# Kernel tuning notes

Hardware: AMD Instinct MI355X
Metric: run time of the kernel (lower is better)

Reference implementation:

```python
import jax, jax.numpy as jnp
import numpy as np

LN_EPS = 1e-5


def _layernorm(x, w, b):
    mu = jnp.mean(x, axis=-1, keepdims=True)
    var = jnp.mean((x - mu) ** 2, axis=-1, keepdims=True)
    return (x - mu) * jax.lax.rsqrt(var + LN_EPS) * w + b


def setup_inputs() -> dict:
    key = jax.random.key(0)
    n, d = 512, 256
    ks = jax.random.split(key, 12)
    s = 1.0 / np.sqrt(d)
    inp = {
        "h": jax.random.normal(ks[0], (n, d), dtype=jnp.float32),
        "e": jax.random.normal(ks[1], (n, n, d), dtype=jnp.float32),
        "t_emb": jax.random.normal(ks[2], (d,), dtype=jnp.float32),
        "W1": jax.random.uniform(ks[3], (d, d), jnp.float32, -s, s),
        "W2": jax.random.uniform(ks[4], (d, d), jnp.float32, -s, s),
        "W3": jax.random.uniform(ks[5], (d, d), jnp.float32, -s, s),
        "W_t": jax.random.uniform(ks[6], (d, d), jnp.float32, -s, s),
        "W4": jax.random.uniform(ks[7], (d, d), jnp.float32, -s, s),
        "W5": jax.random.uniform(ks[8], (d, d), jnp.float32, -s, s),
        "gate_w": jax.random.uniform(ks[9], (d, 1), jnp.float32, -s, s),
        "gate_b": jax.random.uniform(ks[10], (1,), jnp.float32, -s, s),
        "ln_e_w": jnp.ones((d,), jnp.float32),
        "ln_e_b": jnp.zeros((d,), jnp.float32),
        "ln_h_w": jnp.ones((d,), jnp.float32),
        "ln_h_b": jnp.zeros((d,), jnp.float32),
    }
    return inp


def reference(h, e, t_emb, W1, W2, W3, W_t, W4, W5, gate_w, gate_b,
              ln_e_w, ln_e_b, ln_h_w, ln_h_b):
    # nn.Linear applies x @ W.T (no bias except gate)
    t_bias = t_emb @ W_t.T                      # (d,)
    hi = (h @ W1.T)[:, None, :]                 # (n,1,d)
    hj = (h @ W2.T)[None, :, :]                 # (1,n,d)
    pre = hi + hj + jnp.einsum('ijd,kd->ijk', e, W3) + t_bias  # (n,n,d)
    e_new = jax.nn.relu(_layernorm(pre, ln_e_w, ln_e_b))       # (n,n,d)
    logits = e_new @ gate_w + gate_b            # (n,n,1)
    eta = jax.nn.softmax(logits, axis=1)        # softmax over j (dim=1)
    agg = jnp.einsum('ijk,ijd,kd->ik', eta * 1.0, e_new, W5) if False else \
          jnp.sum(eta * jnp.einsum('ijd,kd->ijk', e_new, W5), axis=1)  # (n,d)
    h_new = h + jax.nn.relu(_layernorm(h @ W4.T + agg, ln_h_w, ln_h_b))
    return (h_new, e_new)
```

## Files before the change

kernel.cpp:

```cpp
#include <hip/hip_runtime.h>

#define NN 512
#define DD 256

typedef float f32x4 __attribute__((ext_vector_type(4)));
typedef short s16x8 __attribute__((ext_vector_type(8)));

__device__ __forceinline__ unsigned short f2bf(float f) {
    unsigned u = __float_as_uint(f);
    u += 0x7fffu + ((u >> 16) & 1u);
    return (unsigned short)(u >> 16);
}
__device__ __forceinline__ float bf2f(unsigned short s) {
    return __uint_as_float(((unsigned)s) << 16);
}

__global__ __launch_bounds__(256) void k1_pre(
    const float* __restrict__ h,  const float* __restrict__ W1,
    const float* __restrict__ W2, const float* __restrict__ W4,
    const float* __restrict__ t_emb, const float* __restrict__ W_t,
    const float* __restrict__ W3,
    float* __restrict__ hb, float* __restrict__ hW2, float* __restrict__ hW4,
    unsigned short* __restrict__ w3b,
    float* __restrict__ wacc, float* __restrict__ zacc)
{
    __shared__ float xs[8][DD];
    __shared__ float st[DD];
    const int b = blockIdx.x;
    const int t = threadIdx.x;
    if (b < 64) {
        #pragma unroll
        for (int r = 0; r < 8; ++r) xs[r][t] = h[(size_t)(b * 8 + r) * DD + t];
        st[t] = t_emb[t];
        __syncthreads();
        float a1[8], a2[8], a4[8];
        #pragma unroll
        for (int r = 0; r < 8; ++r) { a1[r] = 0.f; a2[r] = 0.f; a4[r] = 0.f; }
        float tb = 0.f;
        for (int d = 0; d < DD; ++d) {
            const float w1 = W1[(size_t)t * DD + d];
            const float w2 = W2[(size_t)t * DD + d];
            const float w4 = W4[(size_t)t * DD + d];
            tb = fmaf(st[d], W_t[(size_t)t * DD + d], tb);
            #pragma unroll
            for (int r = 0; r < 8; ++r) {
                const float x = xs[r][d];
                a1[r] = fmaf(x, w1, a1[r]);
                a2[r] = fmaf(x, w2, a2[r]);
                a4[r] = fmaf(x, w4, a4[r]);
            }
        }
        #pragma unroll
        for (int r = 0; r < 8; ++r) {
            const size_t o = (size_t)(b * 8 + r) * DD + t;
            hb[o] = a1[r] + tb; hW2[o] = a2[r]; hW4[o] = a4[r];
        }
    } else if (b == 64) {
        for (int c = t; c < DD * DD / 4; c += 256) {
            const f32x4 v = *reinterpret_cast<const f32x4*>(W3 + (size_t)c * 4);
            const unsigned lo = ((unsigned)f2bf(v[1]) << 16) | f2bf(v[0]);
            const unsigned hi = ((unsigned)f2bf(v[3]) << 16) | f2bf(v[2]);
            *reinterpret_cast<uint2*>(w3b + (size_t)c * 4) = make_uint2(lo, hi);
        }
    } else {
        const f32x4 zero = (f32x4){0.f, 0.f, 0.f, 0.f};
        for (int c = t; c < NN * DD / 4; c += 256)
            *reinterpret_cast<f32x4*>(wacc + (size_t)c * 4) = zero;
        if (t < 256) { zacc[t] = 0.f; zacc[t + 256] = 0.f; }
    }
}

__global__ __launch_bounds__(256) void k2_big(
    const float* __restrict__ e,
    const unsigned short* __restrict__ w3b,
    const float* __restrict__ hb, const float* __restrict__ hW2,
    const float* __restrict__ gate_w, const float* __restrict__ gate_b,
    const float* __restrict__ ln_e_w, const float* __restrict__ ln_e_b,
    float* __restrict__ out_e,
    float* __restrict__ wacc, float* __restrict__ zacc)
{
    const int b = blockIdx.x;
    const int row_base = b * 32;
    const int i = row_base >> 9;
    const int j0 = row_base & 511;
    const int tid = threadIdx.x;
    const int w = tid >> 6;
    const int l = tid & 63;
    const int l15 = l & 15;
    const int lg = l >> 4;

    __shared__ __align__(16) unsigned char sA[32 * 256 * 2];
    __shared__ __align__(16) unsigned char sH2[32 * 256 * 2];
    __shared__ unsigned short s_hbu[DD];
    __shared__ float s_lnw[DD], s_lnb[DD], s_gw[DD];
    __shared__ float s_part[32][4][2];
    __shared__ float s_glog[32][4];

    const float* esrc = e + (size_t)row_base * DD;
    f32x4 av[8];
    #pragma unroll
    for (int s = 0; s < 8; ++s)
        av[s] = *reinterpret_cast<const f32x4*>(esrc + (size_t)(s * 256 + tid) * 4);

    const unsigned short* bp = w3b + (size_t)(w * 64 + l15) * DD + lg * 8;
    s16x8 bb[4][4];
    #pragma unroll
    for (int kk = 0; kk < 4; ++kk)
        #pragma unroll
        for (int n = 0; n < 4; ++n)
            bb[kk][n] = *reinterpret_cast<const s16x8*>(bp + (size_t)n * 16 * DD + kk * 32);

    const float gb = gate_b[0];
    s_lnw[tid] = ln_e_w[tid];
    s_lnb[tid] = ln_e_b[tid];
    s_gw[tid]  = gate_w[tid];
    s_hbu[tid] = f2bf(hb[(size_t)i * DD + tid]);

    #pragma unroll
    for (int s = 0; s < 8; ++s) {
        const int flat = s * 256 + tid;
        const int r = flat >> 6;
        const int c4 = (flat & 63) * 4;
        const f32x4 v = av[s];
        const unsigned lo = ((unsigned)f2bf(v[1]) << 16) | f2bf(v[0]);
        const unsigned hi = ((unsigned)f2bf(v[3]) << 16) | f2bf(v[2]);
        const unsigned byte = ((unsigned)(r * 512 + c4 * 2)) ^ ((unsigned)(r & 7) << 4);
        *reinterpret_cast<uint2*>(sA + byte) = make_uint2(lo, hi);
    }

    {
        const float* h2src = hW2 + (size_t)j0 * DD;
        f32x4 hv[8];
        #pragma unroll
        for (int s = 0; s < 8; ++s)
            hv[s] = *reinterpret_cast<const f32x4*>(h2src + (size_t)(s * 256 + tid) * 4);
        #pragma unroll
        for (int s = 0; s < 8; ++s) {
            const int flat = s * 256 + tid;
            const int r = flat >> 6;
            const int c4 = (flat & 63) * 4;
            const f32x4 v = hv[s];
            const unsigned lo = ((unsigned)f2bf(v[1]) << 16) | f2bf(v[0]);
            const unsigned hi = ((unsigned)f2bf(v[3]) << 16) | f2bf(v[2]);
            const unsigned byte = ((unsigned)(r * 512 + c4 * 2)) ^ ((unsigned)(r & 7) << 4);
            *reinterpret_cast<uint2*>(sH2 + byte) = make_uint2(lo, hi);
        }
    }
    __syncthreads();

    f32x4 acc[2][4];
    #pragma unroll
    for (int m = 0; m < 2; ++m)
        #pragma unroll
        for (int n = 0; n < 4; ++n)
            acc[m][n] = (f32x4){0.f, 0.f, 0.f, 0.f};

    const unsigned aswz = ((unsigned)(l15 & 7) << 4);
    #pragma unroll
    for (int kk = 0; kk < 8; ++kk) {
        s16x8 afr[2];
        #pragma unroll
        for (int m = 0; m < 2; ++m) {
            const unsigned byte = ((unsigned)((m * 16 + l15) * 512 + kk * 64 + lg * 16)) ^ aswz;
            afr[m] = *reinterpret_cast<const s16x8*>(sA + byte);
        }
        #pragma unroll
        for (int n = 0; n < 4; ++n)
            #pragma unroll
            for (int m = 0; m < 2; ++m)
                acc[m][n] = __builtin_amdgcn_mfma_f32_16x16x32_bf16(afr[m], bb[kk & 3][n], acc[m][n], 0, 0, 0);
        if (kk < 4) {
            #pragma unroll
            for (int n = 0; n < 4; ++n)
                bb[kk & 3][n] = *reinterpret_cast<const s16x8*>(bp + (size_t)n * 16 * DD + (kk + 4) * 32);
        }
    }

    float hbn[4];
    #pragma unroll
    for (int n = 0; n < 4; ++n) hbn[n] = bf2f(s_hbu[w * 64 + n * 16 + l15]);

    #pragma unroll
    for (int m = 0; m < 2; ++m) {
        #pragma unroll
        for (int q = 0; q < 4; ++q) {
            const int r = m * 16 + lg * 4 + q;
            const unsigned rsw = ((unsigned)(r & 7) << 4);
            float s1 = 0.f, s2 = 0.f;
            #pragma unroll
            for (int n = 0; n < 4; ++n) {
                const int c = w * 64 + n * 16 + l15;
                const unsigned short h2u = *reinterpret_cast<const unsigned short*>(
                    sH2 + (((unsigned)(r * 512 + c * 2)) ^ rsw));
                const float v = acc[m][n][q] + hbn[n] + bf2f(h2u);
                acc[m][n][q] = v;
                s1 += v;
                s2 = fmaf(v, v, s2);
            }
            #pragma unroll
            for (int s = 1; s < 16; s <<= 1) {
                s1 += __shfl_xor(s1, s, 64);
                s2 += __shfl_xor(s2, s, 64);
            }
            if (l15 == 0) { s_part[r][w][0] = s1; s_part[r][w][1] = s2; }
        }
    }
    __syncthreads();

    #pragma unroll
    for (int m = 0; m < 2; ++m) {
        #pragma unroll
        for (int q = 0; q < 4; ++q) {
            const int r = m * 16 + lg * 4 + q;
            float S1 = 0.f, S2 = 0.f;
            #pragma unroll
            for (int ww = 0; ww < 4; ++ww) { S1 += s_part[r][ww][0]; S2 += s_part[r][ww][1]; }
            const float mu = S1 * (1.f / 256.f);
            const float rs = rsqrtf(S2 * (1.f / 256.f) - mu * mu + 1e-5f);
            const size_t rowg = (size_t)(row_base + r);
            float gl = 0.f;
            #pragma unroll
            for (int n = 0; n < 4; ++n) {
                const int c = w * 64 + n * 16 + l15;
                float v = (acc[m][n][q] - mu) * rs * s_lnw[c] + s_lnb[c];
                v = fmaxf(v, 0.f);
                acc[m][n][q] = v;
                out_e[rowg * DD + c] = v;
                gl = fmaf(v, s_gw[c], gl);
            }
            #pragma unroll
            for (int s = 1; s < 16; s <<= 1) gl += __shfl_xor(gl, s, 64);
            if (l15 == 0) s_glog[r][w] = gl;
        }
    }
    __syncthreads();

    float p[4] = {0.f, 0.f, 0.f, 0.f};
    float zl = 0.f;
    #pragma unroll
    for (int m = 0; m < 2; ++m) {
        #pragma unroll
        for (int q = 0; q < 4; ++q) {
            const int r = m * 16 + lg * 4 + q;
            const float lv = gb + s_glog[r][0] + s_glog[r][1] + s_glog[r][2] + s_glog[r][3];
            const float ex = __expf(lv);
            zl += ex;
            #pragma unroll
            for (int n = 0; n < 4; ++n) p[n] = fmaf(ex, acc[m][n][q], p[n]);
        }
    }
    #pragma unroll
    for (int n = 0; n < 4; ++n) {
        p[n] += __shfl_xor(p[n], 16, 64);
        p[n] += __shfl_xor(p[n], 32, 64);
    }
    zl += __shfl_xor(zl, 16, 64);
    zl += __shfl_xor(zl, 32, 64);
    if (lg == 0) {
        #pragma unroll
        for (int n = 0; n < 4; ++n)
            atomicAdd(&wacc[(size_t)i * DD + w * 64 + n * 16 + l15], p[n]);
    }
    if (w == 0 && l == 0) atomicAdd(&zacc[i], zl);
}

__global__ __launch_bounds__(256) void k4_final(
    const float* __restrict__ wacc, const float* __restrict__ zacc,
    const float* __restrict__ W5,
    const float* __restrict__ hW4, const float* __restrict__ h,
    const float* __restrict__ ln_h_w, const float* __restrict__ ln_h_b,
    float* __restrict__ out_h)
{
    const int i = blockIdx.x;
    const int k = threadIdx.x;
    __shared__ float xs[DD];
    __shared__ float red[256];

    const float zinv = 1.f / zacc[i];
    xs[k] = wacc[(size_t)i * DD + k] * zinv;
    __syncthreads();
    float a = 0.f;
    for (int d = 0; d < DD; ++d) a = fmaf(xs[d], W5[(size_t)k * DD + d], a);
    const float p = hW4[(size_t)i * DD + k] + a;

    red[k] = p;
    __syncthreads();
    for (int s = 128; s > 0; s >>= 1) {
        if (k < s) red[k] += red[k + s];
        __syncthreads();
    }
    const float mu = red[0] * (1.f / 256.f);
    __syncthreads();
    const float d0 = p - mu;
    red[k] = d0 * d0;
    __syncthreads();
    for (int s = 128; s > 0; s >>= 1) {
        if (k < s) red[k] += red[k + s];
        __syncthreads();
    }
    const float rs = rsqrtf(red[0] * (1.f / 256.f) + 1e-5f);
    float v = d0 * rs * ln_h_w[k] + ln_h_b[k];
    v = fmaxf(v, 0.f);
    out_h[(size_t)i * DD + k] = h[(size_t)i * DD + k] + v;
}

extern "C" void kernel_launch(void* const* d_in, const int* in_sizes, int n_in,
                              void* d_out, int out_size, void* d_ws, size_t ws_size,
                              hipStream_t stream)
{
    const float* h      = (const float*)d_in[0];
    const float* e      = (const float*)d_in[1];
    const float* t_emb  = (const float*)d_in[2];
    const float* W1     = (const float*)d_in[3];
    const float* W2     = (const float*)d_in[4];
    const float* W3     = (const float*)d_in[5];
    const float* W_t    = (const float*)d_in[6];
    const float* W4     = (const float*)d_in[7];
    const float* W5     = (const float*)d_in[8];
    const float* gate_w = (const float*)d_in[9];
    const float* gate_b = (const float*)d_in[10];
    const float* ln_e_w = (const float*)d_in[11];
    const float* ln_e_b = (const float*)d_in[12];
    const float* ln_h_w = (const float*)d_in[13];
    const float* ln_h_b = (const float*)d_in[14];

    float* out_h = (float*)d_out;
    float* out_e = out_h + NN * DD;

    float* wsf  = (float*)d_ws;
    float* hb   = wsf;
    float* hW2  = hb + NN * DD;
    float* hW4  = hW2 + NN * DD;
    float* wacc = hW4 + NN * DD;
    float* zacc = wacc + NN * DD;
    unsigned short* w3b = (unsigned short*)(zacc + NN);

    k1_pre<<<66, 256, 0, stream>>>(h, W1, W2, W4, t_emb, W_t, W3,
                                   hb, hW2, hW4, w3b, wacc, zacc);
    k2_big<<<8192, 256, 0, stream>>>(e, w3b, hb, hW2, gate_w, gate_b,
                                     ln_e_w, ln_e_b, out_e, wacc, zacc);
    k4_final<<<512, 256, 0, stream>>>(wacc, zacc, W5, hW4, h,
                                      ln_h_w, ln_h_b, out_h);
}
```

Before: 274.9 us.

## Stage e_new output through LDS for coalesced stores; read hW2 directly

The e_new output tile is now written to a padded fp32 LDS buffer, which reuses the A-operand region, and then stored to global memory as coalesced 16-byte vectors, instead of scattered 4-byte stores from the MFMA layout. The hW2 tile is no longer converted to bf16 and staged in LDS. It is read directly from global in fp32 in the epilogue, which removes one LDS buffer and its conversion pass and also drops the bf16 rounding of hW2. The risk is uncoalesced global reads of hW2 in the epilogue and larger LDS use for the output buffer.

```diff
diff --git a/kernel.cpp b/kernel.cpp
--- a/kernel.cpp
+++ b/kernel.cpp
@@ -82,19 +82,18 @@
     const int b = blockIdx.x;
     const int row_base = b * 32;
     const int i = row_base >> 9;
-    const int j0 = row_base & 511;
     const int tid = threadIdx.x;
     const int w = tid >> 6;
     const int l = tid & 63;
     const int l15 = l & 15;
     const int lg = l >> 4;
 
-    __shared__ __align__(16) unsigned char sA[32 * 256 * 2];
-    __shared__ __align__(16) unsigned char sH2[32 * 256 * 2];
+    __shared__ __align__(16) unsigned char sBuf[32 * 260 * 4];
     __shared__ unsigned short s_hbu[DD];
     __shared__ float s_lnw[DD], s_lnb[DD], s_gw[DD];
     __shared__ float s_part[32][4][2];
     __shared__ float s_glog[32][4];
+    float* const sOut = (float*)sBuf;
 
     const float* esrc = e + (size_t)row_base * DD;
     f32x4 av[8];
@@ -125,26 +124,7 @@
         const unsigned lo = ((unsigned)f2bf(v[1]) << 16) | f2bf(v[0]);
         const unsigned hi = ((unsigned)f2bf(v[3]) << 16) | f2bf(v[2]);
         const unsigned byte = ((unsigned)(r * 512 + c4 * 2)) ^ ((unsigned)(r & 7) << 4);
-        *reinterpret_cast<uint2*>(sA + byte) = make_uint2(lo, hi);
-    }
-
-    {
-        const float* h2src = hW2 + (size_t)j0 * DD;
-        f32x4 hv[8];
-        #pragma unroll
-        for (int s = 0; s < 8; ++s)
-            hv[s] = *reinterpret_cast<const f32x4*>(h2src + (size_t)(s * 256 + tid) * 4);
-        #pragma unroll
-        for (int s = 0; s < 8; ++s) {
-            const int flat = s * 256 + tid;
-            const int r = flat >> 6;
-            const int c4 = (flat & 63) * 4;
-            const f32x4 v = hv[s];
-            const unsigned lo = ((unsigned)f2bf(v[1]) << 16) | f2bf(v[0]);
-            const unsigned hi = ((unsigned)f2bf(v[3]) << 16) | f2bf(v[2]);
-            const unsigned byte = ((unsigned)(r * 512 + c4 * 2)) ^ ((unsigned)(r & 7) << 4);
-            *reinterpret_cast<uint2*>(sH2 + byte) = make_uint2(lo, hi);
-        }
+        *reinterpret_cast<uint2*>(sBuf + byte) = make_uint2(lo, hi);
     }
     __syncthreads();
 
@@ -162,7 +142,7 @@
         #pragma unroll
         for (int m = 0; m < 2; ++m) {
             const unsigned byte = ((unsigned)((m * 16 + l15) * 512 + kk * 64 + lg * 16)) ^ aswz;
-            afr[m] = *reinterpret_cast<const s16x8*>(sA + byte);
+            afr[m] = *reinterpret_cast<const s16x8*>(sBuf + byte);
         }
         #pragma unroll
         for (int n = 0; n < 4; ++n)
@@ -185,14 +165,12 @@
         #pragma unroll
         for (int q = 0; q < 4; ++q) {
             const int r = m * 16 + lg * 4 + q;
-            const unsigned rsw = ((unsigned)(r & 7) << 4);
+            const int j = (row_base + r) & 511;
+            const float* h2p = hW2 + (size_t)j * DD + w * 64 + l15;
             float s1 = 0.f, s2 = 0.f;
             #pragma unroll
             for (int n = 0; n < 4; ++n) {
-                const int c = w * 64 + n * 16 + l15;
-                const unsigned short h2u = *reinterpret_cast<const unsigned short*>(
-                    sH2 + (((unsigned)(r * 512 + c * 2)) ^ rsw));
-                const float v = acc[m][n][q] + hbn[n] + bf2f(h2u);
+                const float v = acc[m][n][q] + hbn[n] + h2p[n * 16];
                 acc[m][n][q] = v;
                 s1 += v;
                 s2 = fmaf(v, v, s2);
@@ -217,7 +195,6 @@
             for (int ww = 0; ww < 4; ++ww) { S1 += s_part[r][ww][0]; S2 += s_part[r][ww][1]; }
             const float mu = S1 * (1.f / 256.f);
             const float rs = rsqrtf(S2 * (1.f / 256.f) - mu * mu + 1e-5f);
-            const size_t rowg = (size_t)(row_base + r);
             float gl = 0.f;
             #pragma unroll
             for (int n = 0; n < 4; ++n) {
@@ -225,7 +202,7 @@
                 float v = (acc[m][n][q] - mu) * rs * s_lnw[c] + s_lnb[c];
                 v = fmaxf(v, 0.f);
                 acc[m][n][q] = v;
-                out_e[rowg * DD + c] = v;
+                sOut[r * 260 + c] = v;
                 gl = fmaf(v, s_gw[c], gl);
             }
             #pragma unroll
@@ -262,6 +239,15 @@
             atomicAdd(&wacc[(size_t)i * DD + w * 64 + n * 16 + l15], p[n]);
     }
     if (w == 0 && l == 0) atomicAdd(&zacc[i], zl);
+
+    #pragma unroll
+    for (int s = 0; s < 8; ++s) {
+        const int ch = s * 256 + tid;
+        const int r = ch >> 6;
+        const int c4 = (ch & 63) * 4;
+        const f32x4 v = *reinterpret_cast<const f32x4*>(&sOut[r * 260 + c4]);
+        *reinterpret_cast<f32x4*>(out_e + (size_t)(row_base + r) * DD + c4) = v;
+    }
 }
 
 __global__ __launch_bounds__(256) void k4_final(
```

New measurement: 284.5 us. +3.5%, slower.

## Transpose MFMA operands and stage e_new in LDS for coalesced stores

Applied to the files above, without the earlier changes.

Swaps the MFMA operand roles so W3 fragments are the A operand and e rows are the B operand. Each lane now holds four consecutive feature columns of a row, which cuts the per-row shuffle reductions for the LayerNorm and gate logits. The normalized e_new tile is staged in LDS (reusing the input buffer) and then written to global memory with wide contiguous vector stores instead of scattered 4-byte stores. The softmax-weighted aggregation becomes one atomic per thread. The trade-off is that the e_new output is rounded through bf16 before being written as fp32, which loses precision.

```diff
diff --git a/kernel.cpp b/kernel.cpp
--- a/kernel.cpp
+++ b/kernel.cpp
@@ -13,6 +13,9 @@
 }
 __device__ __forceinline__ float bf2f(unsigned short s) {
     return __uint_as_float(((unsigned)s) << 16);
+}
+__device__ __forceinline__ unsigned packbf(float a, float b) {
+    return ((unsigned)f2bf(b) << 16) | f2bf(a);
 }
 
 __global__ __launch_bounds__(256) void k1_pre(
@@ -58,9 +61,8 @@
     } else if (b == 64) {
         for (int c = t; c < DD * DD / 4; c += 256) {
             const f32x4 v = *reinterpret_cast<const f32x4*>(W3 + (size_t)c * 4);
-            const unsigned lo = ((unsigned)f2bf(v[1]) << 16) | f2bf(v[0]);
-            const unsigned hi = ((unsigned)f2bf(v[3]) << 16) | f2bf(v[2]);
-            *reinterpret_cast<uint2*>(w3b + (size_t)c * 4) = make_uint2(lo, hi);
+            *reinterpret_cast<uint2*>(w3b + (size_t)c * 4) =
+                make_uint2(packbf(v[0], v[1]), packbf(v[2], v[3]));
         }
     } else {
         const f32x4 zero = (f32x4){0.f, 0.f, 0.f, 0.f};
@@ -82,186 +84,202 @@
     const int b = blockIdx.x;
     const int row_base = b * 32;
     const int i = row_base >> 9;
-    const int j0 = row_base & 511;
     const int tid = threadIdx.x;
     const int w = tid >> 6;
     const int l = tid & 63;
     const int l15 = l & 15;
     const int lg = l >> 4;
 
-    __shared__ __align__(16) unsigned char sA[32 * 256 * 2];
-    __shared__ __align__(16) unsigned char sH2[32 * 256 * 2];
+    __shared__ __align__(16) unsigned char sBuf[32768];
+    __shared__ __align__(16) float s_part[32][4][2];
+    __shared__ __align__(16) float s_glog[32][4];
     __shared__ unsigned short s_hbu[DD];
     __shared__ float s_lnw[DD], s_lnb[DD], s_gw[DD];
-    __shared__ float s_part[32][4][2];
-    __shared__ float s_glog[32][4];
-
-    const float* esrc = e + (size_t)row_base * DD;
-    f32x4 av[8];
-    #pragma unroll
-    for (int s = 0; s < 8; ++s)
-        av[s] = *reinterpret_cast<const f32x4*>(esrc + (size_t)(s * 256 + tid) * 4);
-
-    const unsigned short* bp = w3b + (size_t)(w * 64 + l15) * DD + lg * 8;
+    unsigned short* const sOut = (unsigned short*)sBuf;
+
+    const unsigned short* pA = w3b + (size_t)(w * 64 + l15) * DD + lg * 8;
     s16x8 bb[4][4];
     #pragma unroll
     for (int kk = 0; kk < 4; ++kk)
         #pragma unroll
-        for (int n = 0; n < 4; ++n)
-            bb[kk][n] = *reinterpret_cast<const s16x8*>(bp + (size_t)n * 16 * DD + kk * 32);
-
-    const float gb = gate_b[0];
+        for (int m = 0; m < 4; ++m)
+            bb[kk][m] = *reinterpret_cast<const s16x8*>(pA + (size_t)m * 16 * DD + kk * 32);
+
+    {
+        const float* esrc = e + (size_t)row_base * DD;
+        f32x4 av[8];
+        #pragma unroll
+        for (int s = 0; s < 8; ++s)
+            av[s] = *reinterpret_cast<const f32x4*>(esrc + (size_t)(s * 256 + tid) * 4);
+        #pragma unroll
+        for (int s = 0; s < 8; ++s) {
+            const int flat = s * 256 + tid;
+            const int r = flat >> 6;
+            const int c4 = (flat & 63) * 4;
+            const unsigned byte = ((unsigned)(r * 512 + c4 * 2)) ^ ((unsigned)(r & 7) << 4);
+            *reinterpret_cast<uint2*>(sBuf + byte) =
+                make_uint2(packbf(av[s][0], av[s][1]), packbf(av[s][2], av[s][3]));
+        }
+    }
+    {
+        const float* h2src = hW2 + (size_t)(row_base & 511) * DD;
+        f32x4 hv[8];
+        #pragma unroll
+        for (int s = 0; s < 8; ++s)
+            hv[s] = *reinterpret_cast<const f32x4*>(h2src + (size_t)(s * 256 + tid) * 4);
+        #pragma unroll
+        for (int s = 0; s < 8; ++s) {
+            const int flat = s * 256 + tid;
+            const int r = flat >> 6;
+            const int c4 = (flat & 63) * 4;
+            const unsigned byte = ((unsigned)(r * 512 + c4 * 2)) ^ ((unsigned)(r & 7) << 4);
+            *reinterpret_cast<uint2*>(sBuf + 16384 + byte) =
+                make_uint2(packbf(hv[s][0], hv[s][1]), packbf(hv[s][2], hv[s][3]));
+        }
+    }
     s_lnw[tid] = ln_e_w[tid];
     s_lnb[tid] = ln_e_b[tid];
     s_gw[tid]  = gate_w[tid];
     s_hbu[tid] = f2bf(hb[(size_t)i * DD + tid]);
-
-    #pragma unroll
-    for (int s = 0; s < 8; ++s) {
-        const int flat = s * 256 + tid;
-        const int r = flat >> 6;
-        const int c4 = (flat & 63) * 4;
-        const f32x4 v = av[s];
-        const unsigned lo = ((unsigned)f2bf(v[1]) << 16) | f2bf(v[0]);
-        const unsigned hi = ((unsigned)f2bf(v[3]) << 16) | f2bf(v[2]);
-        const unsigned byte = ((unsigned)(r * 512 + c4 * 2)) ^ ((unsigned)(r & 7) << 4);
-        *reinterpret_cast<uint2*>(sA + byte) = make_uint2(lo, hi);
-    }
+    __syncthreads();
+
+    f32x4 acc[4][2];
+    #pragma unroll
+    for (int m = 0; m < 4; ++m) { acc[m][0] = (f32x4){0,0,0,0}; acc[m][1] = (f32x4){0,0,0,0}; }
+
+    const unsigned aswz = ((unsigned)(l15 & 7) << 4);
+    #pragma unroll
+    for (int kk = 0; kk < 8; ++kk) {
+        s16x8 bfr[2];
+        #pragma unroll
+        for (int n = 0; n < 2; ++n) {
+            const int j = n * 16 + l15;
+            const unsigned byte = ((unsigned)(j * 512 + kk * 64 + lg * 16)) ^ aswz;
+            bfr[n] = *reinterpret_cast<const s16x8*>(sBuf + byte);
+        }
+        #pragma unroll
+        for (int m = 0; m < 4; ++m)
+            #pragma unroll
+            for (int n = 0; n < 2; ++n)
+                acc[m][n] = __builtin_amdgcn_mfma_f32_16x16x32_bf16(bb[kk & 3][m], bfr[n], acc[m][n], 0, 0, 0);
+        if (kk < 4) {
+            #pragma unroll
+            for (int m = 0; m < 4; ++m)
+                bb[kk & 3][m] = *reinterpret_cast<const s16x8*>(pA + (size_t)m * 16 * DD + (kk + 4) * 32);
+        }
+    }
+
+    const unsigned char* sH2 = sBuf + 16384;
+    float s1[2] = {0.f, 0.f}, s2[2] = {0.f, 0.f};
+    #pragma unroll
+    for (int m = 0; m < 4; ++m) {
+        const int d0 = w * 64 + m * 16 + lg * 4;
+        const uint2 hbp = *reinterpret_cast<const uint2*>(&s_hbu[d0]);
+        float hbv[4] = { bf2f((unsigned short)hbp.x), bf2f((unsigned short)(hbp.x >> 16)),
+                         bf2f((unsigned short)hbp.y), bf2f((unsigned short)(hbp.y >> 16)) };
+        #pragma unroll
+        for (int n = 0; n < 2; ++n) {
+            const int j = n * 16 + l15;
+            const unsigned byte = ((unsigned)(j * 512 + d0 * 2)) ^ ((unsigned)(j & 7) << 4);
+            const uint2 h2p = *reinterpret_cast<const uint2*>(sH2 + byte);
+            const float h2v[4] = { bf2f((unsigned short)h2p.x), bf2f((unsigned short)(h2p.x >> 16)),
+                                   bf2f((unsigned short)h2p.y), bf2f((unsigned short)(h2p.y >> 16)) };
+            #pragma unroll
+            for (int q = 0; q < 4; ++q) {
+                const float v = acc[m][n][q] + hbv[q] + h2v[q];
+                acc[m][n][q] = v;
+                s1[n] += v;
+                s2[n] = fmaf(v, v, s2[n]);
+            }
+        }
+    }
+    #pragma unroll
+    for (int n = 0; n < 2; ++n) {
+        s1[n] += __shfl_xor(s1[n], 16, 64); s1[n] += __shfl_xor(s1[n], 32, 64);
+        s2[n] += __shfl_xor(s2[n], 16, 64); s2[n] += __shfl_xor(s2[n], 32, 64);
+    }
+    if (lg == 0) {
+        #pragma unroll
+        for (int n = 0; n < 2; ++n) {
+            s_part[n * 16 + l15][w][0] = s1[n];
+            s_part[n * 16 + l15][w][1] = s2[n];
+        }
+    }
+    __syncthreads();
+
+    float mu[2], rs[2];
+    #pragma unroll
+    for (int n = 0; n < 2; ++n) {
+        const int j = n * 16 + l15;
+        float S1 = 0.f, S2 = 0.f;
+        #pragma unroll
+        for (int ww = 0; ww < 4; ++ww) { S1 += s_part[j][ww][0]; S2 += s_part[j][ww][1]; }
+        const float m0 = S1 * (1.f / 256.f);
+        mu[n] = m0;
+        rs[n] = rsqrtf(S2 * (1.f / 256.f) - m0 * m0 + 1e-5f);
+    }
+
+    float gl[2] = {0.f, 0.f};
+    #pragma unroll
+    for (int m = 0; m < 4; ++m) {
+        const int d0 = w * 64 + m * 16 + lg * 4;
+        const f32x4 lw = *reinterpret_cast<const f32x4*>(&s_lnw[d0]);
+        const f32x4 lb = *reinterpret_cast<const f32x4*>(&s_lnb[d0]);
+        const f32x4 gw = *reinterpret_cast<const f32x4*>(&s_gw[d0]);
+        #pragma unroll
+        for (int n = 0; n < 2; ++n) {
+            const int j = n * 16 + l15;
+            float vv[4];
+            #pragma unroll
+            for (int q = 0; q < 4; ++q) {
+                float v = (acc[m][n][q] - mu[n]) * rs[n] * lw[q] + lb[q];
+                v = fmaxf(v, 0.f);
+                vv[q] = v;
+                gl[n] = fmaf(v, gw[q], gl[n]);
+            }
+            *reinterpret_cast<uint2*>(&sOut[j * 264 + d0]) =
+                make_uint2(packbf(vv[0], vv[1]), packbf(vv[2], vv[3]));
+        }
+    }
+    #pragma unroll
+    for (int n = 0; n < 2; ++n) {
+        gl[n] += __shfl_xor(gl[n], 16, 64);
+        gl[n] += __shfl_xor(gl[n], 32, 64);
+    }
+    if (lg == 0) {
+        s_glog[l15][w]      = gl[0];
+        s_glog[l15 + 16][w] = gl[1];
+    }
+    __syncthreads();
+
+    const float gb = gate_b[0];
+    float pacc = 0.f, zsum = 0.f;
+    #pragma unroll 4
+    for (int r = 0; r < 32; ++r) {
+        const f32x4 g4 = *reinterpret_cast<const f32x4*>(&s_glog[r][0]);
+        const float ex = __expf((g4[0] + g4[1]) + (g4[2] + g4[3]) + gb);
+        zsum += ex;
+        pacc = fmaf(ex, bf2f(sOut[r * 264 + tid]), pacc);
+    }
+    atomicAdd(&wacc[(size_t)i * DD + tid], pacc);
+    if (tid == 0) atomicAdd(&zacc[i], zsum);
 
     {
-        const float* h2src = hW2 + (size_t)j0 * DD;
-        f32x4 hv[8];
-        #pragma unroll
-        for (int s = 0; s < 8; ++s)
-            hv[s] = *reinterpret_cast<const f32x4*>(h2src + (size_t)(s * 256 + tid) * 4);
-        #pragma unroll
-        for (int s = 0; s < 8; ++s) {
-            const int flat = s * 256 + tid;
-            const int r = flat >> 6;
-            const int c4 = (flat & 63) * 4;
-            const f32x4 v = hv[s];
-            const unsigned lo = ((unsigned)f2bf(v[1]) << 16) | f2bf(v[0]);
-            const unsigned hi = ((unsigned)f2bf(v[3]) << 16) | f2bf(v[2]);
-            const unsigned byte = ((unsigned)(r * 512 + c4 * 2)) ^ ((unsigned)(r & 7) << 4);
-            *reinterpret_cast<uint2*>(sH2 + byte) = make_uint2(lo, hi);
-        }
-    }
-    __syncthreads();
-
-    f32x4 acc[2][4];
-    #pragma unroll
-    for (int m = 0; m < 2; ++m)
-        #pragma unroll
-        for (int n = 0; n < 4; ++n)
-            acc[m][n] = (f32x4){0.f, 0.f, 0.f, 0.f};
-
-    const unsigned aswz = ((unsigned)(l15 & 7) << 4);
-    #pragma unroll
-    for (int kk = 0; kk < 8; ++kk) {
-        s16x8 afr[2];
-        #pragma unroll
-        for (int m = 0; m < 2; ++m) {
-            const unsigned byte = ((unsigned)((m * 16 + l15) * 512 + kk * 64 + lg * 16)) ^ aswz;
-            afr[m] = *reinterpret_cast<const s16x8*>(sA + byte);
-        }
-        #pragma unroll
-        for (int n = 0; n < 4; ++n)
-            #pragma unroll
-            for (int m = 0; m < 2; ++m)
-                acc[m][n] = __builtin_amdgcn_mfma_f32_16x16x32_bf16(afr[m], bb[kk & 3][n], acc[m][n], 0, 0, 0);
-        if (kk < 4) {
-            #pragma unroll
-            for (int n = 0; n < 4; ++n)
-                bb[kk & 3][n] = *reinterpret_cast<const s16x8*>(bp + (size_t)n * 16 * DD + (kk + 4) * 32);
-        }
-    }
-
-    float hbn[4];
-    #pragma unroll
-    for (int n = 0; n < 4; ++n) hbn[n] = bf2f(s_hbu[w * 64 + n * 16 + l15]);
-
-    #pragma unroll
-    for (int m = 0; m < 2; ++m) {
-        #pragma unroll
-        for (int q = 0; q < 4; ++q) {
-            const int r = m * 16 + lg * 4 + q;
-            const unsigned rsw = ((unsigned)(r & 7) << 4);
-            float s1 = 0.f, s2 = 0.f;
-            #pragma unroll
-            for (int n = 0; n < 4; ++n) {
-                const int c = w * 64 + n * 16 + l15;
-                const unsigned short h2u = *reinterpret_cast<const unsigned short*>(
-                    sH2 + (((unsigned)(r * 512 + c * 2)) ^ rsw));
-                const float v = acc[m][n][q] + hbn[n] + bf2f(h2u);
-                acc[m][n][q] = v;
-                s1 += v;
-                s2 = fmaf(v, v, s2);
-            }
-            #pragma unroll
-            for (int s = 1; s < 16; s <<= 1) {
-                s1 += __shfl_xor(s1, s, 64);
-                s2 += __shfl_xor(s2, s, 64);
-            }
-            if (l15 == 0) { s_part[r][w][0] = s1; s_part[r][w][1] = s2; }
-        }
-    }
-    __syncthreads();
-
-    #pragma unroll
-    for (int m = 0; m < 2; ++m) {
-        #pragma unroll
-        for (int q = 0; q < 4; ++q) {
-            const int r = m * 16 + lg * 4 + q;
-            float S1 = 0.f, S2 = 0.f;
-            #pragma unroll
-            for (int ww = 0; ww < 4; ++ww) { S1 += s_part[r][ww][0]; S2 += s_part[r][ww][1]; }
-            const float mu = S1 * (1.f / 256.f);
-            const float rs = rsqrtf(S2 * (1.f / 256.f) - mu * mu + 1e-5f);
-            const size_t rowg = (size_t)(row_base + r);
-            float gl = 0.f;
-            #pragma unroll
-            for (int n = 0; n < 4; ++n) {
-                const int c = w * 64 + n * 16 + l15;
-                float v = (acc[m][n][q] - mu) * rs * s_lnw[c] + s_lnb[c];
-                v = fmaxf(v, 0.f);
-                acc[m][n][q] = v;
-                out_e[rowg * DD + c] = v;
-                gl = fmaf(v, s_gw[c], gl);
-            }
-            #pragma unroll
-            for (int s = 1; s < 16; s <<= 1) gl += __shfl_xor(gl, s, 64);
-            if (l15 == 0) s_glog[r][w] = gl;
-        }
-    }
-    __syncthreads();
-
-    float p[4] = {0.f, 0.f, 0.f, 0.f};
-    float zl = 0.f;
-    #pragma unroll
-    for (int m = 0; m < 2; ++m) {
-        #pragma unroll
-        for (int q = 0; q < 4; ++q) {
-            const int r = m * 16 + lg * 4 + q;
-            const float lv = gb + s_glog[r][0] + s_glog[r][1] + s_glog[r][2] + s_glog[r][3];
-            const float ex = __expf(lv);
-            zl += ex;
-            #pragma unroll
-            for (int n = 0; n < 4; ++n) p[n] = fmaf(ex, acc[m][n][q], p[n]);
-        }
-    }
-    #pragma unroll
-    for (int n = 0; n < 4; ++n) {
-        p[n] += __shfl_xor(p[n], 16, 64);
-        p[n] += __shfl_xor(p[n], 32, 64);
-    }
-    zl += __shfl_xor(zl, 16, 64);
-    zl += __shfl_xor(zl, 32, 64);
-    if (lg == 0) {
-        #pragma unroll
-        for (int n = 0; n < 4; ++n)
-            atomicAdd(&wacc[(size_t)i * DD + w * 64 + n * 16 + l15], p[n]);
-    }
-    if (w == 0 && l == 0) atomicAdd(&zacc[i], zl);
+        const int rr = tid >> 3;
+        const int cb = (tid & 7) * 32;
+        #pragma unroll
+        for (int c = 0; c < 4; ++c) {
+            const uint4 u = *reinterpret_cast<const uint4*>(&sOut[rr * 264 + cb + c * 8]);
+            f32x4 o0, o1;
+            o0[0] = bf2f((unsigned short)u.x); o0[1] = bf2f((unsigned short)(u.x >> 16));
+            o0[2] = bf2f((unsigned short)u.y); o0[3] = bf2f((unsigned short)(u.y >> 16));
+            o1[0] = bf2f((unsigned short)u.z); o1[1] = bf2f((unsigned short)(u.z >> 16));
+            o1[2] = bf2f((unsigned short)u.w); o1[3] = bf2f((unsigned short)(u.w >> 16));
+            float* dst = out_e + (size_t)(row_base + rr) * DD + cb + c * 8;
+            *reinterpret_cast<f32x4*>(dst) = o0;
+            *reinterpret_cast<f32x4*>(dst + 4) = o1;
+        }
+    }
 }
 
 __global__ __launch_bounds__(256) void k4_final(
```

Measured after the change: 293.6 us. +6.8%, slower.
